# Optimization experiments

Measured on AMD Instinct MI355X. Metric: run time of the kernel, lower is better.

The kernel has to match this reference:

```python
import jax, jax.numpy as jnp
import numpy as np

LEAKY_SLOPE = 0.01
BN_EPS = 1e-5


def _local_conv(x, w, b, stride):
    # x: [B,C,H,W]; w: [1,O,C,OH,OW,K] (K = kh*kw, kh==kw); b: [1,O,OH,OW]
    sh, sw = stride
    _, O, C, oh, ow, K = w.shape
    k = int(round(K ** 0.5))
    # gather unfold patches: torch .unfold(2,kh,dh).unfold(3,kw,dw) -> last dim ordered (i major, j minor)
    patches = jnp.stack(
        [x[:, :, i:i + sh * oh:sh, j:j + sw * ow:sw] for i in range(k) for j in range(k)],
        axis=-1)  # [B,C,oh,ow,K]
    out = jnp.einsum('bchwk,ochwk->bohw', patches, w[0])
    return out + b  # b broadcasts [1,O,OH,OW]


def _bn_train(x, gamma, beta):
    # BatchNorm2d in training mode: biased batch statistics over (N,H,W)
    m = jnp.mean(x, axis=(0, 2, 3), keepdims=True)
    v = jnp.var(x, axis=(0, 2, 3), keepdims=True)
    return gamma[None, :, None, None] * (x - m) * jax.lax.rsqrt(v + BN_EPS) + beta[None, :, None, None]


def _lrelu(x):
    return jnp.where(x >= 0, x, LEAKY_SLOPE * x)


def _pad1(x):
    return jnp.pad(x, ((0, 0), (0, 0), (1, 1), (1, 1)))


def setup_inputs() -> dict:
    key = jax.random.key(0)
    ks = jax.random.split(key, 16)
    B = 8192
    inp = {
        'image': jax.random.normal(ks[0], (B, 10, 9, 1), jnp.float32),
        'conv1_w': jax.random.normal(ks[1], (64, 1, 2, 2), jnp.float32) * 0.5,
        'conv1_b': jax.random.normal(ks[2], (64,), jnp.float32) * 0.1,
        'lc1_w': jax.random.normal(ks[3], (1, 16, 64, 10, 5, 9), jnp.float32) * 0.05,
        'lc1_b': jax.random.normal(ks[4], (1, 16, 10, 5), jnp.float32) * 0.1,
        'lc2_w': jax.random.normal(ks[5], (1, 8, 16, 11, 6, 4), jnp.float32) * 0.1,
        'lc2_b': jax.random.normal(ks[6], (1, 8, 11, 6), jnp.float32) * 0.1,
        'lc3_w': jax.random.normal(ks[7], (1, 8, 8, 12, 4, 4), jnp.float32) * 0.1,
        'lc3_b': jax.random.normal(ks[8], (1, 8, 12, 4), jnp.float32) * 0.1,
        'gamma1': jax.random.normal(ks[9], (16,), jnp.float32) * 0.1 + 1.0,
        'beta1': jax.random.normal(ks[10], (16,), jnp.float32) * 0.1,
        'gamma2': jax.random.normal(ks[11], (8,), jnp.float32) * 0.1 + 1.0,
        'beta2': jax.random.normal(ks[12], (8,), jnp.float32) * 0.1,
        'gamma3': jax.random.normal(ks[13], (8,), jnp.float32) * 0.1 + 1.0,
        'beta3': jax.random.normal(ks[14], (8,), jnp.float32) * 0.1,
    }
    return inp


def reference(image, conv1_w, conv1_b, lc1_w, lc1_b, lc2_w, lc2_b, lc3_w, lc3_b,
              gamma1, beta1, gamma2, beta2, gamma3, beta3):
    x = jnp.transpose(image, (0, 3, 1, 2))  # [B,1,10,9]
    # Conv2d kernel 2, padding='same' (torch pads extra on right/bottom for even kernels)
    x = jax.lax.conv_general_dilated(
        x, conv1_w, window_strides=(1, 1), padding=[(0, 1), (0, 1)],
        dimension_numbers=('NCHW', 'OIHW', 'NCHW'))
    x = x + conv1_b[None, :, None, None]
    x = _lrelu(x)
    x = _pad1(x)                               # [B,64,12,11]
    x = _local_conv(x, lc1_w, lc1_b, (1, 2))   # [B,16,10,5]
    x = _lrelu(x)
    x = _bn_train(x, gamma1, beta1)
    x = _pad1(x)                               # [B,16,12,7]
    x = _local_conv(x, lc2_w, lc2_b, (1, 1))   # [B,8,11,6]
    x = _lrelu(x)
    x = _bn_train(x, gamma2, beta2)
    x = _pad1(x)                               # [B,8,13,8]
    x = _local_conv(x, lc3_w, lc3_b, (1, 2))   # [B,8,12,4]
    x = _lrelu(x)
    x = _bn_train(x, gamma3, beta3)
    return x.reshape(x.shape[0], -1)           # [B,384]
```

## Files before the change

### kernel.cpp

```cpp
#include <hip/hip_runtime.h>


typedef float  f32x4 __attribute__((ext_vector_type(4)));
typedef float  f32x2 __attribute__((ext_vector_type(2)));
typedef short  bf16x8 __attribute__((ext_vector_type(8)));

union FR  { int4 i4; bf16x8 bf; unsigned u[4]; };

#define LRELU(v) fmaxf((v), 0.01f * (v))

static __device__ inline unsigned bfr(float f) {
    unsigned u = __float_as_uint(f);
    return (u + 0x7fffu + ((u >> 16) & 1u)) >> 16;
}
static __device__ inline unsigned short bfr16(float f) { return (unsigned short)bfr(f); }
static __device__ inline float ubf(unsigned lo16) { return __uint_as_float(lo16 << 16); }

#if __has_builtin(__builtin_elementwise_fma)
static __device__ inline f32x2 pk_fma(f32x2 a, f32x2 b, f32x2 c) { return __builtin_elementwise_fma(a, b, c); }
#else
static __device__ inline f32x2 pk_fma(f32x2 a, f32x2 b, f32x2 c) { return a * b + c; }
#endif
static __device__ inline f32x2 pk_lrelu(f32x2 v) {
#if __has_builtin(__builtin_elementwise_max)
    return __builtin_elementwise_max(v, v * 0.01f);
#else
    f32x2 r; r.x = LRELU(v.x); r.y = LRELU(v.y); return r;
#endif
}
static __device__ inline float aload(float* p) {
    return __hip_atomic_load(p, __ATOMIC_RELAXED, __HIP_MEMORY_SCOPE_AGENT);
}

union PrepSM { float imgP[16][110]; float wt[9216]; };

__global__ __launch_bounds__(256) void kprep(
    const float* __restrict__ imgp,
    const float* __restrict__ cw,
    const float* __restrict__ cb,
    const float* __restrict__ lw1,
    unsigned* __restrict__ x1u,
    int4* __restrict__ afg1, float* __restrict__ stats,
    int nA, int doAux)
{
    __shared__ PrepSM sm;
    const int bx = blockIdx.x, tid = threadIdx.x;

    if (bx < nA) {
        const int sb = bx * 16;
        for (int e = tid; e < 1760; e += 256) ((float*)sm.imgP)[e] = 0.0f;
        __syncthreads();
        for (int e = tid; e < 1440; e += 256) {
            int s = e / 90, hw = e - s * 90;
            int r = hw / 9, c = hw - r * 9;
            sm.imgP[s][r * 10 + c] = imgp[(size_t)sb * 90 + e];
        }
        __syncthreads();

        const int chp = tid & 31, sidx = tid >> 5;
        const int ch0 = 2 * chp;
        f32x2 w00 = {cw[ch0 * 4 + 0], cw[ch0 * 4 + 4]};
        f32x2 w01 = {cw[ch0 * 4 + 1], cw[ch0 * 4 + 5]};
        f32x2 w10 = {cw[ch0 * 4 + 2], cw[ch0 * 4 + 6]};
        f32x2 w11 = {cw[ch0 * 4 + 3], cw[ch0 * 4 + 7]};
        f32x2 bb  = {cb[ch0], cb[ch0 + 1]};

        #pragma unroll
        for (int ss = 0; ss < 2; ++ss) {
            const int s = sidx + 8 * ss;
            const float* ip = sm.imgP[s];
            unsigned* dst = x1u + (size_t)(sb + s) * 2880 + chp;
            #pragma unroll 2
            for (int r = 0; r < 10; ++r) {
                #pragma unroll
                for (int c = 0; c < 9; ++c) {
                    f32x2 v = bb;
                    v = pk_fma((f32x2)ip[r * 10 + c],      w00, v);
                    v = pk_fma((f32x2)ip[r * 10 + c + 1],  w01, v);
                    v = pk_fma((f32x2)ip[r * 10 + c + 10], w10, v);
                    v = pk_fma((f32x2)ip[r * 10 + c + 11], w11, v);
                    v = pk_lrelu(v);
                    dst[(r * 9 + c) * 32] = bfr(v.x) | (bfr(v.y) << 16);
                }
            }
        }
        return;
    }
    if (!doAux) return;

    const int b2 = bx - nA;
    if (b2 < 50) {
        const int pos = b2;
        for (int e = tid; e < 9216; e += 256) {
            int pair = e / 9, t = e - 9 * pair;
            sm.wt[e] = lw1[pair * 450 + pos * 9 + t];
        }
        __syncthreads();
        for (int e = tid; e < 1152; e += 256) {
            int l = e & 63, ht = e >> 6;
            int h = (ht >= 9) ? 1 : 0, t = ht - 9 * h;
            int q = l >> 4, o = l & 15;
            unsigned uu[4];
            #pragma unroll
            for (int p = 0; p < 4; ++p) {
                int c0 = 32 * h + 8 * q + 2 * p;
                float a0 = sm.wt[(o * 64 + c0) * 9 + t];
                float a1 = sm.wt[(o * 64 + c0 + 1) * 9 + t];
                uu[p] = bfr(a0) | (bfr(a1) << 16);
            }
            int4 st = { (int)uu[0], (int)uu[1], (int)uu[2], (int)uu[3] };
            afg1[pos * 1152 + e] = st;
        }
    } else if (tid < 64) stats[tid] = 0.0f;
}

__global__ __launch_bounds__(256) void k1_lc1(
    const int4* __restrict__ x1v,
    const int4* __restrict__ afg,
    const float* __restrict__ lb,
    unsigned short* __restrict__ y1b,
    float* __restrict__ stats,
    int sampOff)
{
    __shared__ int4  AfL[1152];
    __shared__ float bl[16];
    __shared__ float red[32];

    const int pos = blockIdx.y;
    const int oh = pos / 5, ow = pos % 5;
    const int tid = threadIdx.x;
    const int wv = tid >> 6, lane = tid & 63;
    const int lane15 = lane & 15, q = lane >> 4;

    for (int e = tid; e < 1152; e += 256) AfL[e] = afg[pos * 1152 + e];
    if (tid < 16) bl[tid] = lb[tid * 50 + pos];
    if (tid < 32) red[tid] = 0.0f;
    __syncthreads();

    const int sLoc = blockIdx.x * 256 + wv * 64;
    const int sAbs = sampOff + sLoc;

    int sOff[4];
    #pragma unroll
    for (int g = 0; g < 4; ++g)
        sOff[g] = (sLoc + g * 16 + lane15) * 720 + q;

    f32x4 acc[4];
    #pragma unroll
    for (int g = 0; g < 4; ++g) acc[g] = (f32x4){0.f, 0.f, 0.f, 0.f};

    #pragma unroll
    for (int t = 0; t < 9; ++t) {
        const int ti = t / 3, tj = t % 3;
        const int r = oh + ti - 1, c2 = 2 * ow + tj - 1;
        if (r >= 0 && r < 10 && c2 >= 0 && c2 < 9) {
            const int hw8 = (r * 9 + c2) * 8;
            #pragma unroll
            for (int h = 0; h < 2; ++h) {
                FR fa; fa.i4 = AfL[(h * 9 + t) * 64 + lane];
                #pragma unroll
                for (int g = 0; g < 4; ++g) {
                    FR fb; fb.i4 = x1v[sOff[g] + hw8 + h * 4];
                    acc[g] = __builtin_amdgcn_mfma_f32_16x16x32_bf16(fa.bf, fb.bf, acc[g], 0, 0, 0);
                }
            }
        }
    }

    float so[4] = {0, 0, 0, 0}, sq[4] = {0, 0, 0, 0};
    #pragma unroll
    for (int g = 0; g < 4; ++g)
        #pragma unroll
        for (int r = 0; r < 4; ++r) {
            int o = q * 4 + r;
            float v = acc[g][r] + bl[o];
            v = LRELU(v);
            y1b[(size_t)(o * 50 + pos) * 8192 + sAbs + g * 16 + lane15] = bfr16(v);
            so[r] += v; sq[r] += v * v;
        }
    #pragma unroll
    for (int r = 0; r < 4; ++r) {
        #pragma unroll
        for (int m = 1; m < 16; m <<= 1) {
            so[r] += __shfl_xor(so[r], m, 16);
            sq[r] += __shfl_xor(sq[r], m, 16);
        }
        if (lane15 == 0) {
            int o = q * 4 + r;
            atomicAdd(&red[o], so[r]);
            atomicAdd(&red[16 + o], sq[r]);
        }
    }
    __syncthreads();
    if (tid < 32) atomicAdd(&stats[tid], red[tid]);
}

__global__ __launch_bounds__(256) void k2_lc2(
    const unsigned short* __restrict__ y1b,
    const float* __restrict__ lw2, const float* __restrict__ lb2,
    const float* __restrict__ g1, const float* __restrict__ be1,
    unsigned short* __restrict__ y2b, float* __restrict__ stats)
{
    __shared__ float wld[512];
    __shared__ float a1[16], b1[16], bl[8], red[16];

    const int unit = blockIdx.x;
    const int pos = unit >> 3, chunk = unit & 7;
    const int oh = pos / 6, ow = pos % 6;
    const int tid = threadIdx.x, lane = tid & 63;

    if (tid < 128) {
        const float* src = lw2 + tid * 264 + pos * 4;
        int o = tid >> 4, c = tid & 15;
        #pragma unroll
        for (int k = 0; k < 4; k++) wld[c * 32 + k * 8 + o] = src[k];
    }
    if (tid < 16) {
        float m = aload(&stats[tid]) * (1.0f / 409600.0f);
        float v = aload(&stats[16 + tid]) * (1.0f / 409600.0f) - m * m;
        float a = g1[tid] * rsqrtf(v + 1e-5f);
        a1[tid] = a; b1[tid] = be1[tid] - a * m;
        if (tid < 8) bl[tid] = lb2[tid * 66 + pos];
        red[tid] = 0.0f;
    }
    __syncthreads();

    int base[4]; float kmv[4];
    #pragma unroll
    for (int i = 0; i < 2; i++)
        #pragma unroll
        for (int j = 0; j < 2; j++) {
            int r = oh + i - 1, c2 = ow + j - 1;
            bool ok = (r >= 0 && r < 10 && c2 >= 0 && c2 < 5);
            int rc = min(max(r, 0), 9), cc2 = min(max(c2, 0), 4);
            base[i * 2 + j] = rc * 5 + cc2;
            kmv[i * 2 + j] = ok ? 1.0f : 0.0f;
        }

    const int sb = chunk * 1024 + tid * 4;
    float acc[8][4];
    #pragma unroll
    for (int o = 0; o < 8; o++)
        #pragma unroll
        for (int s = 0; s < 4; s++) acc[o][s] = bl[o];

    #pragma unroll 1
    for (int c = 0; c < 16; c++) {
        float av = a1[c], bv = b1[c];
        float p[4][4];
        #pragma unroll
        for (int t = 0; t < 4; t++) {
            float ap = av * kmv[t], bp = bv * kmv[t];
            uint2 U = *(const uint2*)(y1b + (size_t)(c * 50 + base[t]) * 8192 + sb);
            p[t][0] = fmaf(ap, ubf(U.x & 0xffffu), bp);
            p[t][1] = fmaf(ap, __uint_as_float(U.x & 0xffff0000u), bp);
            p[t][2] = fmaf(ap, ubf(U.y & 0xffffu), bp);
            p[t][3] = fmaf(ap, __uint_as_float(U.y & 0xffff0000u), bp);
        }
        const float4* wr = (const float4*)&wld[c * 32];
        #pragma unroll
        for (int t = 0; t < 4; t++) {
            float4 wa = wr[t * 2], wb = wr[t * 2 + 1];
            #pragma unroll
            for (int s = 0; s < 4; s++) {
                float pv = p[t][s];
                acc[0][s] += wa.x * pv; acc[1][s] += wa.y * pv;
                acc[2][s] += wa.z * pv; acc[3][s] += wa.w * pv;
                acc[4][s] += wb.x * pv; acc[5][s] += wb.y * pv;
                acc[6][s] += wb.z * pv; acc[7][s] += wb.w * pv;
            }
        }
    }

    #pragma unroll
    for (int o = 0; o < 8; o++) {
        float v0 = LRELU(acc[o][0]), v1 = LRELU(acc[o][1]);
        float v2 = LRELU(acc[o][2]), v3 = LRELU(acc[o][3]);
        uint2 st = { bfr(v0) | (bfr(v1) << 16), bfr(v2) | (bfr(v3) << 16) };
        *(uint2*)(y2b + (size_t)(o * 66 + pos) * 8192 + sb) = st;
        float sv = v0 + v1 + v2 + v3;
        float sqv = v0 * v0 + v1 * v1 + v2 * v2 + v3 * v3;
        #pragma unroll
        for (int m = 32; m > 0; m >>= 1) {
            sv  += __shfl_xor(sv, m, 64);
            sqv += __shfl_xor(sqv, m, 64);
        }
        if (lane == 0) { atomicAdd(&red[o], sv); atomicAdd(&red[8 + o], sqv); }
    }
    __syncthreads();
    if (tid < 16) atomicAdd(&stats[32 + tid], red[tid]);
}

__global__ __launch_bounds__(256) void k3_lc3(
    const unsigned short* __restrict__ y2b,
    const float* __restrict__ lw3, const float* __restrict__ lb3,
    const float* __restrict__ g2, const float* __restrict__ be2,
    unsigned short* __restrict__ y3b, float* __restrict__ stats)
{
    __shared__ float wld[256];
    __shared__ float a2[8], b2[8], bl[8], red[16];

    const int unit = blockIdx.x;
    const int pos = unit >> 3, chunk = unit & 7;
    const int oh = pos >> 2, ow = pos & 3;
    const int tid = threadIdx.x, lane = tid & 63;

    if (tid < 64) {
        const float* src = lw3 + tid * 192 + pos * 4;
        int o = tid >> 3, c = tid & 7;
        #pragma unroll
        for (int k = 0; k < 4; k++) wld[c * 32 + k * 8 + o] = src[k];
    }
    if (tid < 16) {
        if (tid < 8) {
            float m = aload(&stats[32 + tid]) * (1.0f / 540672.0f);
            float v = aload(&stats[40 + tid]) * (1.0f / 540672.0f) - m * m;
            float a = g2[tid] * rsqrtf(v + 1e-5f);
            a2[tid] = a; b2[tid] = be2[tid] - a * m;
            bl[tid] = lb3[tid * 48 + pos];
        }
        red[tid] = 0.0f;
    }
    __syncthreads();

    int base[4]; float kmv[4];
    #pragma unroll
    for (int i = 0; i < 2; i++)
        #pragma unroll
        for (int j = 0; j < 2; j++) {
            int r = oh + i - 1, c2 = 2 * ow + j - 1;
            bool ok = (r >= 0 && r < 11 && c2 >= 0 && c2 < 6);
            int rc = min(max(r, 0), 10), cc2 = min(max(c2, 0), 5);
            base[i * 2 + j] = rc * 6 + cc2;
            kmv[i * 2 + j] = ok ? 1.0f : 0.0f;
        }

    const int sb = chunk * 1024 + tid * 4;
    float acc[8][4];
    #pragma unroll
    for (int o = 0; o < 8; o++)
        #pragma unroll
        for (int s = 0; s < 4; s++) acc[o][s] = bl[o];

    #pragma unroll 1
    for (int c = 0; c < 8; c++) {
        float av = a2[c], bv = b2[c];
        float p[4][4];
        #pragma unroll
        for (int t = 0; t < 4; t++) {
            float ap = av * kmv[t], bp = bv * kmv[t];
            uint2 U = *(const uint2*)(y2b + (size_t)(c * 66 + base[t]) * 8192 + sb);
            p[t][0] = fmaf(ap, ubf(U.x & 0xffffu), bp);
            p[t][1] = fmaf(ap, __uint_as_float(U.x & 0xffff0000u), bp);
            p[t][2] = fmaf(ap, ubf(U.y & 0xffffu), bp);
            p[t][3] = fmaf(ap, __uint_as_float(U.y & 0xffff0000u), bp);
        }
        const float4* wr = (const float4*)&wld[c * 32];
        #pragma unroll
        for (int t = 0; t < 4; t++) {
            float4 wa = wr[t * 2], wb = wr[t * 2 + 1];
            #pragma unroll
            for (int s = 0; s < 4; s++) {
                float pv = p[t][s];
                acc[0][s] += wa.x * pv; acc[1][s] += wa.y * pv;
                acc[2][s] += wa.z * pv; acc[3][s] += wa.w * pv;
                acc[4][s] += wb.x * pv; acc[5][s] += wb.y * pv;
                acc[6][s] += wb.z * pv; acc[7][s] += wb.w * pv;
            }
        }
    }

    #pragma unroll
    for (int o = 0; o < 8; o++) {
        float v0 = LRELU(acc[o][0]), v1 = LRELU(acc[o][1]);
        float v2 = LRELU(acc[o][2]), v3 = LRELU(acc[o][3]);
        uint2 st = { bfr(v0) | (bfr(v1) << 16), bfr(v2) | (bfr(v3) << 16) };
        *(uint2*)(y3b + (size_t)(o * 48 + pos) * 8192 + sb) = st;
        float sv = v0 + v1 + v2 + v3;
        float sqv = v0 * v0 + v1 * v1 + v2 * v2 + v3 * v3;
        #pragma unroll
        for (int m = 32; m > 0; m >>= 1) {
            sv  += __shfl_xor(sv, m, 64);
            sqv += __shfl_xor(sqv, m, 64);
        }
        if (lane == 0) { atomicAdd(&red[o], sv); atomicAdd(&red[8 + o], sqv); }
    }
    __syncthreads();
    if (tid < 16) atomicAdd(&stats[48 + tid], red[tid]);
}

__global__ __launch_bounds__(256) void k4_out(
    const unsigned short* __restrict__ y3b,
    const float* __restrict__ g3, const float* __restrict__ be3,
    float* __restrict__ stats, float* __restrict__ out)
{
    __shared__ unsigned short tile[64][66];
    __shared__ float a3[8], b3[8];
    const int unit = blockIdx.x;
    const int tid = threadIdx.x;
    const int chunkS = unit & 31, yy = unit >> 5;
    const int ftile = yy >> 2, sub = yy & 3;
    const int fbase = ftile * 64;
    const int sbase = chunkS * 256 + sub * 64;

    if (tid < 8) {
        float m = aload(&stats[48 + tid]) * (1.0f / 393216.0f);
        float v = aload(&stats[56 + tid]) * (1.0f / 393216.0f) - m * m;
        float a = g3[tid] * rsqrtf(v + 1e-5f);
        a3[tid] = a; b3[tid] = be3[tid] - a * m;
    }
    __syncthreads();

    #pragma unroll
    for (int rep = 0; rep < 16; rep++) {
        int idx = rep * 256 + tid;
        int f = idx >> 6, s = idx & 63;
        tile[f][s] = y3b[(size_t)(fbase + f) * 8192 + sbase + s];
    }
    __syncthreads();
    #pragma unroll
    for (int rep = 0; rep < 16; rep++) {
        int idx = rep * 256 + tid;
        int s = idx >> 6, f = idx & 63;
        int ff = fbase + f;
        int o = ff / 48;
        float x = ubf((unsigned)tile[f][s]);
        out[(size_t)(sbase + s) * 384 + ff] = a3[o] * x + b3[o];
    }
}

extern "C" void kernel_launch(void* const* d_in, const int* in_sizes, int n_in,
                              void* d_out, int out_size, void* d_ws, size_t ws_size,
                              hipStream_t stream) {
    const float* image   = (const float*)d_in[0];
    const float* conv1_w = (const float*)d_in[1];
    const float* conv1_b = (const float*)d_in[2];
    const float* lc1_w   = (const float*)d_in[3];
    const float* lc1_b   = (const float*)d_in[4];
    const float* lc2_w   = (const float*)d_in[5];
    const float* lc2_b   = (const float*)d_in[6];
    const float* lc3_w   = (const float*)d_in[7];
    const float* lc3_b   = (const float*)d_in[8];
    const float* gamma1  = (const float*)d_in[9];
    const float* beta1   = (const float*)d_in[10];
    const float* gamma2  = (const float*)d_in[11];
    const float* beta2   = (const float*)d_in[12];
    const float* gamma3  = (const float*)d_in[13];
    const float* beta3   = (const float*)d_in[14];
    float* outp = (float*)d_out;

    char* wsb = (char*)d_ws;
    float*          stats = (float*)wsb;
    unsigned short* y1b   = (unsigned short*)(wsb + 1024);
    int4*           afg1  = (int4*)(wsb + 13108224);
    char*           x1reg = wsb + 14029824;
    unsigned short* y2b   = (unsigned short*)(wsb + 14029824);
    unsigned short* y3b   = (unsigned short*)(wsb + 22680576);

    const size_t bytesPerSamp = 11520;
    int nPass = 1;
    if (ws_size < 14029824ul + 8192ul * bytesPerSamp) nPass = 2;
    if (ws_size < 14029824ul + 4096ul * bytesPerSamp) nPass = 4;
    if (ws_size < 14029824ul + 2048ul * bytesPerSamp) nPass = 8;
    const int spp = 8192 / nPass;
    const int nA  = spp / 16;

    unsigned*   x1u = (unsigned*)x1reg;
    const int4* x1v = (const int4*)x1reg;

    for (int p = 0; p < nPass; ++p) {
        const float* imgp = image + (size_t)p * spp * 90;
        kprep<<<dim3(p == 0 ? nA + 51 : nA), dim3(256), 0, stream>>>(
            imgp, conv1_w, conv1_b, lc1_w, x1u, afg1, stats, nA, p == 0 ? 1 : 0);
        k1_lc1<<<dim3(spp / 256, 50), dim3(256), 0, stream>>>(
            x1v, afg1, lc1_b, y1b, stats, p * spp);
    }
    k2_lc2<<<dim3(528), dim3(256), 0, stream>>>(y1b, lc2_w, lc2_b,
                                                gamma1, beta1, y2b, stats);
    k3_lc3<<<dim3(384), dim3(256), 0, stream>>>(y2b, lc3_w, lc3_b,
                                                gamma2, beta2, y3b, stats);
    k4_out<<<dim3(768), dim3(256), 0, stream>>>(y3b, gamma3, beta3, stats, outp);
}
```

Before: 221.1 us.

## Store conv1 activations position-major and remap lc1 blocks for XCD locality

The conv1 output buffer changes from sample-major order (all 90 positions × 64 channels per sample) to position/half-major slabs, so each MFMA B-fragment load reads 64 contiguous bytes across neighbouring samples instead of striding 11520 bytes between samples. The lc1 grid is flattened to 1D with a block-id remap that spreads sample chunks across the 8 XCDs while keeping the same position's blocks together, which is meant to improve L2 reuse of the shared weights. In exchange, kprep's stores become scattered, with large strides per sample and position, so write coalescing there may suffer.

Result: faster. 203.0 us (-8.2%).

```diff
diff --git a/kernel.cpp b/kernel.cpp
--- a/kernel.cpp
+++ b/kernel.cpp
@@ -41,7 +41,7 @@
     const float* __restrict__ lw1,
     unsigned* __restrict__ x1u,
     int4* __restrict__ afg1, float* __restrict__ stats,
-    int nA, int doAux)
+    int nA, int doAux, int spp)
 {
     __shared__ PrepSM sm;
     const int bx = blockIdx.x, tid = threadIdx.x;
@@ -59,6 +59,7 @@
 
         const int chp = tid & 31, sidx = tid >> 5;
         const int ch0 = 2 * chp;
+        const int h = chp >> 4, chpos = chp & 15;
         f32x2 w00 = {cw[ch0 * 4 + 0], cw[ch0 * 4 + 4]};
         f32x2 w01 = {cw[ch0 * 4 + 1], cw[ch0 * 4 + 5]};
         f32x2 w10 = {cw[ch0 * 4 + 2], cw[ch0 * 4 + 6]};
@@ -69,7 +70,7 @@
         for (int ss = 0; ss < 2; ++ss) {
             const int s = sidx + 8 * ss;
             const float* ip = sm.imgP[s];
-            unsigned* dst = x1u + (size_t)(sb + s) * 2880 + chp;
+            unsigned* dst = x1u + ((size_t)h * spp + (sb + s)) * 16 + chpos;
             #pragma unroll 2
             for (int r = 0; r < 10; ++r) {
                 #pragma unroll
@@ -80,7 +81,7 @@
                     v = pk_fma((f32x2)ip[r * 10 + c + 10], w10, v);
                     v = pk_fma((f32x2)ip[r * 10 + c + 11], w11, v);
                     v = pk_lrelu(v);
-                    dst[(r * 9 + c) * 32] = bfr(v.x) | (bfr(v.y) << 16);
+                    dst[(size_t)(r * 9 + c) * 2 * spp * 16] = bfr(v.x) | (bfr(v.y) << 16);
                 }
             }
         }
@@ -120,13 +121,18 @@
     const float* __restrict__ lb,
     unsigned short* __restrict__ y1b,
     float* __restrict__ stats,
-    int sampOff)
+    int sampOff, int spp, int nc)
 {
     __shared__ int4  AfL[1152];
     __shared__ float bl[16];
     __shared__ float red[32];
 
-    const int pos = blockIdx.y;
+    int pos, chunk;
+    {
+        int id = blockIdx.x;
+        if (nc >= 8) { int k8 = id & 7; int r = id >> 3; pos = r % 50; chunk = (r / 50) * 8 + k8; }
+        else         { pos = id % 50; chunk = id / 50; }
+    }
     const int oh = pos / 5, ow = pos % 5;
     const int tid = threadIdx.x;
     const int wv = tid >> 6, lane = tid & 63;
@@ -137,13 +143,14 @@
     if (tid < 32) red[tid] = 0.0f;
     __syncthreads();
 
-    const int sLoc = blockIdx.x * 256 + wv * 64;
+    const int sLoc = chunk * 256 + wv * 64;
     const int sAbs = sampOff + sLoc;
-
-    int sOff[4];
+    const int spp4 = spp * 4;
+
+    int base_g[4];
     #pragma unroll
     for (int g = 0; g < 4; ++g)
-        sOff[g] = (sLoc + g * 16 + lane15) * 720 + q;
+        base_g[g] = (sLoc + g * 16 + lane15) * 4 + q;
 
     f32x4 acc[4];
     #pragma unroll
@@ -154,13 +161,14 @@
         const int ti = t / 3, tj = t % 3;
         const int r = oh + ti - 1, c2 = 2 * ow + tj - 1;
         if (r >= 0 && r < 10 && c2 >= 0 && c2 < 9) {
-            const int hw8 = (r * 9 + c2) * 8;
+            const int hw = r * 9 + c2;
             #pragma unroll
             for (int h = 0; h < 2; ++h) {
                 FR fa; fa.i4 = AfL[(h * 9 + t) * 64 + lane];
+                const int slabBase = (hw * 2 + h) * spp4;
                 #pragma unroll
                 for (int g = 0; g < 4; ++g) {
-                    FR fb; fb.i4 = x1v[sOff[g] + hw8 + h * 4];
+                    FR fb; fb.i4 = x1v[slabBase + base_g[g]];
                     acc[g] = __builtin_amdgcn_mfma_f32_16x16x32_bf16(fa.bf, fb.bf, acc[g], 0, 0, 0);
                 }
             }
@@ -464,6 +472,7 @@
     if (ws_size < 14029824ul + 2048ul * bytesPerSamp) nPass = 8;
     const int spp = 8192 / nPass;
     const int nA  = spp / 16;
+    const int nc  = spp / 256;
 
     unsigned*   x1u = (unsigned*)x1reg;
     const int4* x1v = (const int4*)x1reg;
@@ -471,9 +480,9 @@
     for (int p = 0; p < nPass; ++p) {
         const float* imgp = image + (size_t)p * spp * 90;
         kprep<<<dim3(p == 0 ? nA + 51 : nA), dim3(256), 0, stream>>>(
-            imgp, conv1_w, conv1_b, lc1_w, x1u, afg1, stats, nA, p == 0 ? 1 : 0);
-        k1_lc1<<<dim3(spp / 256, 50), dim3(256), 0, stream>>>(
-            x1v, afg1, lc1_b, y1b, stats, p * spp);
+            imgp, conv1_w, conv1_b, lc1_w, x1u, afg1, stats, nA, p == 0 ? 1 : 0, spp);
+        k1_lc1<<<dim3(50 * nc), dim3(256), 0, stream>>>(
+            x1v, afg1, lc1_b, y1b, stats, p * spp, spp, nc);
     }
     k2_lc2<<<dim3(528), dim3(256), 0, stream>>>(y1b, lc2_w, lc2_b,
                                                 gamma1, beta1, y2b, stats);
```
